# Optimization experiments

Hardware: AMD Instinct MI355X
Metric: run time of the kernel (lower is better)

## Reference

```python
import jax, jax.numpy as jnp
import numpy as np

N_QUBIT = 20
N_LAYER = 50
FEAT = 128
BATCH = 128
N_NODES = BATCH * N_QUBIT * (N_LAYER + 1)  # 130560
N_EDGES = 524288
VOCAB = N_QUBIT * (N_LAYER + 1) + 1  # 1021
NEG_SLOPE = 0.01


def setup_inputs() -> dict:
    key = jax.random.key(0)
    ks = jax.random.split(key, 32)
    s = 0.05
    x = jax.random.randint(ks[0], (N_NODES,), 0, VOCAB, dtype=jnp.int64 if jax.config.read('jax_enable_x64') else jnp.int32)
    edge_index = jax.random.randint(ks[1], (2, N_EDGES), 0, N_NODES, dtype=x.dtype)
    emb = (jax.random.normal(ks[2], (VOCAB, FEAT), jnp.float32) * s).at[0].set(0.0)  # padding_idx=0
    gcn_w = jax.random.normal(ks[3], (5, FEAT, FEAT), jnp.float32) * s
    gcn_b = jnp.zeros((5, FEAT), jnp.float32)
    mlp_dims = [(2 * FEAT, 2 * FEAT), (2 * FEAT, FEAT), (FEAT, FEAT), (FEAT, FEAT // 2), (FEAT // 2, FEAT // 2), (FEAT // 2, 1)]
    mlp = {}
    for i, (din, dout) in enumerate(mlp_dims):
        mlp[f'mw{i}'] = jax.random.normal(ks[4 + i], (din, dout), jnp.float32) * s
        mlp[f'mb{i}'] = jnp.zeros((dout,), jnp.float32)
    return dict(x=x, edge_index=edge_index, emb=emb, gcn_w=gcn_w, gcn_b=gcn_b, **mlp)


def _leaky(v):
    return jnp.where(v >= 0, v, NEG_SLOPE * v)


def _gcn(h, src, dst, W, b):
    # PyG GCNConv: h' = D^-1/2 (A+I) D^-1/2 (h W) + b, flow src -> dst
    n = h.shape[0]
    hw = h @ W
    loops = jnp.arange(n, dtype=src.dtype)
    s2 = jnp.concatenate([src, loops])
    d2 = jnp.concatenate([dst, loops])
    deg = jax.ops.segment_sum(jnp.ones(s2.shape[0], hw.dtype), d2, num_segments=n)
    dinv = jnp.where(deg > 0, jax.lax.rsqrt(deg), 0.0)
    norm = dinv[s2] * dinv[d2]  # [E+N]
    out = jax.ops.segment_sum(hw[s2] * norm[:, None], d2, num_segments=n)
    return out + b


def reference(x, edge_index, emb, gcn_w, gcn_b, mw0, mb0, mw1, mb1, mw2, mb2, mw3, mb3, mw4, mb4, mw5, mb5):
    src, dst = edge_index[0], edge_index[1]
    h = emb[x]  # [N, f]
    for i in range(4):
        h = _leaky(_gcn(h, src, dst, gcn_w[i], gcn_b[i])) + h
    h = _gcn(h, src, dst, gcn_w[4], gcn_b[4]) + h
    n, f = N_QUBIT, FEAT
    h = h.reshape(-1, n * (N_LAYER + 1), f)[:, :n, :]  # [B, n, f]
    b = h.shape[0]
    # cartesian pairs (i, j): concat(h_i, h_j) -> [B, n, n, 2f]
    xi = jnp.broadcast_to(h[:, :, None, :], (b, n, n, f))
    xj = jnp.broadcast_to(h[:, None, :, :], (b, n, n, f))
    p = jnp.concatenate([xi, xj], axis=-1)
    p = _leaky(p @ mw0 + mb0)
    p = _leaky(p @ mw1 + mb1)
    p = _leaky(p @ mw2 + mb2)
    p = _leaky(p @ mw3 + mb3)
    p = _leaky(p @ mw4 + mb4)
    p = (p @ mw5 + mb5)[..., 0]  # [B, n, n]
    p = (p + jnp.swapaxes(p, -1, -2)) / 2
    return p.reshape(-1, n * n)
```

## Files before the change

### kernel.cpp

```cpp
#include <hip/hip_runtime.h>
#include <hip/hip_bf16.h>

#define NQ 20
#define NLAY 51
#define FEAT 128
#define BATCH 128
#define NN (BATCH * NQ * NLAY)
#define NE 524288
#define NPAIR (BATCH * NQ * NQ)
#define NB (NN / 256)
#define VOCAB 1021

typedef _Float16 half8 __attribute__((ext_vector_type(8)));
typedef float floatx4 __attribute__((ext_vector_type(4)));
typedef unsigned int uint;

__device__ __forceinline__ float lrelu(float v) { return v >= 0.f ? v : 0.01f * v; }

__device__ __forceinline__ uint packhl(float v) {
    _Float16 h = (_Float16)v;
    _Float16 l = (_Float16)(v - (float)h);
    union { _Float16 f; unsigned short u; } hb, lb;
    hb.f = h; lb.f = l;
    return (uint)hb.u | ((uint)lb.u << 16);
}

__device__ __forceinline__ void unpack8(uint4 a, uint4 b, half8& hi, half8& lo) {
    union { uint u[4]; half8 h; } H, L;
    H.u[0] = __builtin_amdgcn_perm(a.y, a.x, 0x05040100u);
    H.u[1] = __builtin_amdgcn_perm(a.w, a.z, 0x05040100u);
    H.u[2] = __builtin_amdgcn_perm(b.y, b.x, 0x05040100u);
    H.u[3] = __builtin_amdgcn_perm(b.w, b.z, 0x05040100u);
    L.u[0] = __builtin_amdgcn_perm(a.y, a.x, 0x07060302u);
    L.u[1] = __builtin_amdgcn_perm(a.w, a.z, 0x07060302u);
    L.u[2] = __builtin_amdgcn_perm(b.y, b.x, 0x07060302u);
    L.u[3] = __builtin_amdgcn_perm(b.w, b.z, 0x07060302u);
    hi = H.h;
    lo = L.h;
}

__global__ void k_count(const int* __restrict__ dst, int* __restrict__ cnt) {
    int e = blockIdx.x * 256 + threadIdx.x;
    atomicAdd(&cnt[dst[e]], 1);
}

__global__ void k_offsets(const int* __restrict__ cnt, const int* __restrict__ x,
                          int* __restrict__ offs, float* __restrict__ dinv,
                          int4* __restrict__ meta, int* __restrict__ cursor,
                          int* __restrict__ flag1, int* __restrict__ idmap) {
    __shared__ int sm[256];
    __shared__ int sbase;
    int t = threadIdx.x, g = blockIdx.x * 256 + t;
    int v = cnt[g];
    sm[t] = v;
    __syncthreads();
    for (int s = 1; s < 256; s <<= 1) {
        int add = (t >= s) ? sm[t - s] : 0;
        __syncthreads();
        sm[t] += add;
        __syncthreads();
    }
    if (t == 255) sbase = atomicAdd(cursor, sm[255]);
    __syncthreads();
    int off = sbase + sm[t] - v;
    float di = rsqrtf((float)(v + 1));
    offs[g] = off;
    dinv[g] = di;
    meta[g] = make_int4(off, v, __float_as_int(di), x[g]);
    if (g % (NQ * NLAY) < NQ) flag1[g] = 1;
    if (g < 1024) idmap[g] = min(g, VOCAB - 1);
}

__global__ void k_fill(const int* __restrict__ src, const int* __restrict__ dst,
                       const int* __restrict__ offs, int* __restrict__ fill,
                       const float* __restrict__ dinv, const int* __restrict__ x,
                       int2* __restrict__ csre, int2* __restrict__ csre0,
                       int* __restrict__ flag1) {
    int e = blockIdx.x * 256 + threadIdx.x;
    int d = dst[e];
    int s = src[e];
    int pos = offs[d] + atomicAdd(&fill[d], 1);
    int wb = __float_as_int(dinv[s] * dinv[d]);
    csre[pos] = make_int2(s, wb);
    csre0[pos] = make_int2(x[s], wb);
    if (d % (NQ * NLAY) < NQ) flag1[s] = 1;
}

__global__ void k_s1pass(const int* __restrict__ flagI, const int4* __restrict__ meta,
                         const int2* __restrict__ csre, int* __restrict__ cur,
                         int* __restrict__ listO, int4* __restrict__ recO,
                         int* __restrict__ flagO) {
    __shared__ int sm[256];
    __shared__ int sbase;
    int t = threadIdx.x, g = blockIdx.x * 256 + t;
    int v = flagI[g];
    sm[t] = v;
    __syncthreads();
    for (int s = 1; s < 256; s <<= 1) {
        int add = (t >= s) ? sm[t - s] : 0;
        __syncthreads();
        sm[t] += add;
        __syncthreads();
    }
    if (t == 255) sbase = atomicAdd(cur, sm[255]);
    __syncthreads();
    if (v) {
        int slot = sbase + sm[t] - 1;
        listO[slot] = g;
        int4 m = meta[g];
        float di = __int_as_float(m.z);
        int dc = min(m.y, 6);
        int2 eb[6];
#pragma unroll
        for (int j = 0; j < 6; j++) eb[j] = (j < dc) ? csre[m.x + j] : make_int2(0, 0);
        int4* r = recO + (size_t)slot * 4;
        r[0] = make_int4(g + 1, m.y, __float_as_int(di * di), m.x);
        r[1] = make_int4(eb[0].x, eb[0].y, eb[1].x, eb[1].y);
        r[2] = make_int4(eb[2].x, eb[2].y, eb[3].x, eb[3].y);
        r[3] = make_int4(eb[4].x, eb[4].y, eb[5].x, eb[5].y);
        if (flagO) {
            flagO[g] = 1;
            for (int e = 0; e < m.y; e++) flagO[csre[m.x + e].x] = 1;
        }
    }
}

__global__ void k_rec0(const int4* __restrict__ meta, const int2* __restrict__ csre,
                       int4* __restrict__ rec0) {
    int q = blockIdx.x * 256 + threadIdx.x;
    if (q >= BATCH * NQ) return;
    int b = q / NQ, i = q - b * NQ;
    int node = b * (NQ * NLAY) + i;
    int4 m = meta[node];
    float di = __int_as_float(m.z);
    int dc = min(m.y, 6);
    int2 eb[6];
#pragma unroll
    for (int j = 0; j < 6; j++) eb[j] = (j < dc) ? csre[m.x + j] : make_int2(0, 0);
    int4* r = rec0 + (size_t)q * 4;
    r[0] = make_int4(node + 1, m.y, __float_as_int(di * di), m.x);
    r[1] = make_int4(eb[0].x, eb[0].y, eb[1].x, eb[1].y);
    r[2] = make_int4(eb[2].x, eb[2].y, eb[3].x, eb[3].y);
    r[3] = make_int4(eb[4].x, eb[4].y, eb[5].x, eb[5].y);
}

#define OFF_GCN 0
#define OFF_P0  81920
#define OFF_M1  147456
#define OFF_M2  180224
#define OFF_M3  196608
#define OFF_M4  204800
#define TS_TOTAL 208896

__global__ void k_tsplit_all(const float* __restrict__ gw, const float* __restrict__ mw0,
                             const float* __restrict__ mw1, const float* __restrict__ mw2,
                             const float* __restrict__ mw3, const float* __restrict__ mw4,
                             _Float16* __restrict__ hi, _Float16* __restrict__ lo) {
    int idx = blockIdx.x * 256 + threadIdx.x;
    const float* src;
    int K, N, rel;
    bool p0 = false;
    if (idx < OFF_P0) {
        int L = (idx - OFF_GCN) >> 14; rel = (idx - OFF_GCN) & 16383;
        src = gw + L * 16384; K = 128; N = 128;
    } else if (idx < OFF_M1) {
        rel = idx - OFF_P0; src = mw0; K = 128; N = 512; p0 = true;
    } else if (idx < OFF_M2) {
        rel = idx - OFF_M1;  src = mw1; K = 256; N = 128;
    } else if (idx < OFF_M3) {
        rel = idx - OFF_M2;  src = mw2; K = 128; N = 128;
    } else if (idx < OFF_M4) {
        rel = idx - OFF_M3;  src = mw3; K = 128; N = 64;
    } else {
        rel = idx - OFF_M4;  src = mw4; K = 64;  N = 64;
    }
    int kblks = K >> 5;
    int j = rel & 7;
    int lane = (rel >> 3) & 63;
    int t2 = rel >> 9;
    int kblk = t2 % kblks;
    int ntile = t2 / kblks;
    int col = ntile * 16 + (lane & 15);
    int k = kblk * 32 + ((lane >> 4) << 3) + j;
    float f;
    if (p0) {
        f = (col < 256) ? src[k * 256 + col] : src[(k + 128) * 256 + (col - 256)];
    } else {
        f = src[k * N + col];
    }
    _Float16 h = (_Float16)f;
    hi[idx] = h;
    lo[idx] = (_Float16)(f - (float)h);
}

template <int NT_N, bool LEAKY, bool BIAS, bool P0SPLIT, bool FUSEA, bool GATHA, bool LISTM>
__launch_bounds__(256, 2)
__global__ void hgemm(const float* __restrict__ A,
                      const float* __restrict__ FA, const float* __restrict__ FB,
                      const _Float16* __restrict__ Bh, const _Float16* __restrict__ Bl,
                      const float* __restrict__ bias,
                      float* __restrict__ C, float* __restrict__ C2,
                      int N, int K, const int* __restrict__ gmap,
                      const int* __restrict__ listm) {
    if (LISTM) {
        if ((unsigned)listm[blockIdx.x * 128] >= (unsigned)NN) return;
    }
    const int KB = K >> 5;
    const int lane = threadIdx.x & 63;
    const int wid = threadIdx.x >> 6;
    const int lm = lane & 15, lq = lane >> 4;
    const int m0 = blockIdx.x * 128 + wid * 32;
    const int n0t = blockIdx.y * NT_N;

    const float* arow[2];
    const float* brow[2];
#pragma unroll
    for (int mt = 0; mt < 2; mt++) {
        int row = m0 + mt * 16 + lm;
        if (FUSEA) {
            int b = row / (NQ * NQ);
            int rr = row - b * (NQ * NQ);
            int i = rr / NQ;
            int j = rr - i * NQ;
            arow[mt] = FA + (size_t)(b * NQ + i) * 256;
            brow[mt] = FB + (size_t)(b * NQ + j) * 256;
        } else if (GATHA) {
            arow[mt] = A + (size_t)gmap[row] * K;
        } else if (LISTM) {
            int lr = listm[row];
            lr = ((unsigned)lr < (unsigned)NN) ? lr : 0;
            arow[mt] = A + (size_t)lr * K;
        } else {
            arow[mt] = A + (size_t)row * K;
        }
    }

    floatx4 acc[2][NT_N];
#pragma unroll
    for (int mt = 0; mt < 2; mt++)
#pragma unroll
        for (int nt = 0; nt < NT_N; nt++) acc[mt][nt] = (floatx4)0.f;

    for (int kb = 0; kb < KB; kb++) {
        const int k0 = kb * 32 + lq * 8;
        half8 ahi[2], alo[2];
#pragma unroll
        for (int mt = 0; mt < 2; mt++) {
            floatx4 av0, av1;
            if (FUSEA) {
                floatx4 fa0 = *(const floatx4*)(arow[mt] + k0);
                floatx4 fa1 = *(const floatx4*)(arow[mt] + k0 + 4);
                floatx4 fb0 = *(const floatx4*)(brow[mt] + k0);
                floatx4 fb1 = *(const floatx4*)(brow[mt] + k0 + 4);
#pragma unroll
                for (int q = 0; q < 4; q++) {
                    av0[q] = lrelu(fa0[q] + fb0[q]);
                    av1[q] = lrelu(fa1[q] + fb1[q]);
                }
            } else {
                av0 = *(const floatx4*)(arow[mt] + k0);
                av1 = *(const floatx4*)(arow[mt] + k0 + 4);
            }
#pragma unroll
            for (int q = 0; q < 4; q++) {
                _Float16 h0 = (_Float16)av0[q];
                ahi[mt][q] = h0;
                alo[mt][q] = (_Float16)(av0[q] - (float)h0);
                _Float16 h1 = (_Float16)av1[q];
                ahi[mt][4 + q] = h1;
                alo[mt][4 + q] = (_Float16)(av1[q] - (float)h1);
            }
        }
#pragma unroll
        for (int nt = 0; nt < NT_N; nt++) {
            size_t boff = (((size_t)(n0t + nt) * KB + kb) * 64 + lane) * 8;
            half8 bhi = *(const half8*)(Bh + boff);
            half8 blo = *(const half8*)(Bl + boff);
#pragma unroll
            for (int mt = 0; mt < 2; mt++) {
                acc[mt][nt] = __builtin_amdgcn_mfma_f32_16x16x32_f16(ahi[mt], bhi, acc[mt][nt], 0, 0, 0);
                acc[mt][nt] = __builtin_amdgcn_mfma_f32_16x16x32_f16(ahi[mt], blo, acc[mt][nt], 0, 0, 0);
                acc[mt][nt] = __builtin_amdgcn_mfma_f32_16x16x32_f16(alo[mt], bhi, acc[mt][nt], 0, 0, 0);
            }
        }
    }

    int strow[2][4];
    bool svalid[2][4];
#pragma unroll
    for (int mt = 0; mt < 2; mt++)
#pragma unroll
        for (int r = 0; r < 4; r++) {
            int mlog = m0 + mt * 16 + lq * 4 + r;
            if (LISTM) {
                int sr = listm[mlog];
                svalid[mt][r] = (unsigned)sr < (unsigned)NN;
                strow[mt][r] = svalid[mt][r] ? sr : 0;
            } else {
                svalid[mt][r] = true;
                strow[mt][r] = mlog;
            }
        }

#pragma unroll
    for (int nt = 0; nt < NT_N; nt++) {
        int col = (n0t + nt) * 16 + lm;
        float bv = (BIAS || P0SPLIT) ? bias[col < 256 ? col : 0] : 0.f;
#pragma unroll
        for (int mt = 0; mt < 2; mt++) {
#pragma unroll
            for (int r = 0; r < 4; r++) {
                if (!svalid[mt][r]) continue;
                int row = strow[mt][r];
                float val = acc[mt][nt][r];
                if (P0SPLIT) {
                    if (col < 256) C[(size_t)row * 256 + col] = val + bv;
                    else C2[(size_t)row * 256 + col - 256] = val;
                } else {
                    if (BIAS) val += bv;
                    if (LEAKY) val = lrelu(val);
                    C[(size_t)row * N + col] = val;
                }
            }
        }
    }
}

template <bool LEAKY, bool FINAL>
__launch_bounds__(256, 8)
__global__ void k_lagg(const float* __restrict__ in, float* __restrict__ outp,
                       const int4* __restrict__ rec, const int2* __restrict__ csre,
                       const int* __restrict__ cntp, int fixcnt,
                       const _Float16* __restrict__ Bh, const _Float16* __restrict__ Bl,
                       const float* __restrict__ bias) {
    int lcnt = cntp ? *cntp : fixcnt;
    int sbase = blockIdx.x * 16;
    if (sbase >= lcnt) return;
    __shared__ uint X[16][132];
    int tid = threadIdx.x;
    int sl = tid & 31;
    int grp = tid >> 5;
    const float4* in4 = (const float4*)in;
    {
        int lrow0 = grp * 2;
        int p0i = sbase + lrow0, p1i = p0i + 1;
        bool val0 = p0i < lcnt, val1 = p1i < lcnt;
        const int4* r0p = rec + (size_t)(val0 ? p0i : 0) * 4;
        const int4* r1p = rec + (size_t)(val1 ? p1i : 0) * 4;
        int4 hd0 = r0p[0], ea0 = r0p[1], eb0 = r0p[2], ec0 = r0p[3];
        int4 hd1 = r1p[0], ea1 = r1p[1], eb1 = r1p[2], ec1 = r1p[3];
        int n0 = hd0.x - 1;
        int n1 = hd1.x - 1;
        float s20 = __int_as_float(hd0.z), s21 = __int_as_float(hd1.z);
        float4 v0  = in4[(size_t)n0 * 32 + sl];
        float4 v1  = in4[(size_t)n1 * 32 + sl];
        float4 u00 = in4[(size_t)ea0.x * 32 + sl];
        float4 u01 = in4[(size_t)ea0.z * 32 + sl];
        float4 u02 = in4[(size_t)eb0.x * 32 + sl];
        float4 u03 = in4[(size_t)eb0.z * 32 + sl];
        float4 u04 = in4[(size_t)ec0.x * 32 + sl];
        float4 u05 = in4[(size_t)ec0.z * 32 + sl];
        float4 u10 = in4[(size_t)ea1.x * 32 + sl];
        float4 u11 = in4[(size_t)ea1.z * 32 + sl];
        float4 u12 = in4[(size_t)eb1.x * 32 + sl];
        float4 u13 = in4[(size_t)eb1.z * 32 + sl];
        float4 u14 = in4[(size_t)ec1.x * 32 + sl];
        float4 u15 = in4[(size_t)ec1.z * 32 + sl];
        float w00 = __int_as_float(ea0.y), w01 = __int_as_float(ea0.w);
        float w02 = __int_as_float(eb0.y), w03 = __int_as_float(eb0.w);
        float w04 = __int_as_float(ec0.y), w05 = __int_as_float(ec0.w);
        float w10 = __int_as_float(ea1.y), w11 = __int_as_float(ea1.w);
        float w12 = __int_as_float(eb1.y), w13 = __int_as_float(eb1.w);
        float w14 = __int_as_float(ec1.y), w15 = __int_as_float(ec1.w);
        float a0x = v0.x * s20 + u00.x * w00 + u01.x * w01 + u02.x * w02 + u03.x * w03 + u04.x * w04 + u05.x * w05;
        float a0y = v0.y * s20 + u00.y * w00 + u01.y * w01 + u02.y * w02 + u03.y * w03 + u04.y * w04 + u05.y * w05;
        float a0z = v0.z * s20 + u00.z * w00 + u01.z * w01 + u02.z * w02 + u03.z * w03 + u04.z * w04 + u05.z * w05;
        float a0w = v0.w * s20 + u00.w * w00 + u01.w * w01 + u02.w * w02 + u03.w * w03 + u04.w * w04 + u05.w * w05;
        float a1x = v1.x * s21 + u10.x * w10 + u11.x * w11 + u12.x * w12 + u13.x * w13 + u14.x * w14 + u15.x * w15;
        float a1y = v1.y * s21 + u10.y * w10 + u11.y * w11 + u12.y * w12 + u13.y * w13 + u14.y * w14 + u15.y * w15;
        float a1z = v1.z * s21 + u10.z * w10 + u11.z * w11 + u12.z * w12 + u13.z * w13 + u14.z * w14 + u15.z * w15;
        float a1w = v1.w * s21 + u10.w * w10 + u11.w * w11 + u12.w * w12 + u13.w * w13 + u14.w * w14 + u15.w * w15;
        int deg0 = val0 ? hd0.y : 0, deg1 = val1 ? hd1.y : 0;
        int dm = max(deg0, deg1);
        if (dm > 6) {
            int off0 = hd0.w, off1 = hd1.w;
            int d0c = max(deg0 - 1, 0), d1c = max(deg1 - 1, 0);
            for (int e = 6; e < dm; e += 6) {
                int2 e00 = csre[off0 + min(e,     d0c)];
                int2 e01 = csre[off0 + min(e + 1, d0c)];
                int2 e02 = csre[off0 + min(e + 2, d0c)];
                int2 e03 = csre[off0 + min(e + 3, d0c)];
                int2 e04 = csre[off0 + min(e + 4, d0c)];
                int2 e05 = csre[off0 + min(e + 5, d0c)];
                int2 e10 = csre[off1 + min(e,     d1c)];
                int2 e11 = csre[off1 + min(e + 1, d1c)];
                int2 e12 = csre[off1 + min(e + 2, d1c)];
                int2 e13 = csre[off1 + min(e + 3, d1c)];
                int2 e14 = csre[off1 + min(e + 4, d1c)];
                int2 e15 = csre[off1 + min(e + 5, d1c)];
                float4 x00 = in4[(size_t)e00.x * 32 + sl];
                float4 x01 = in4[(size_t)e01.x * 32 + sl];
                float4 x02 = in4[(size_t)e02.x * 32 + sl];
                float4 x03 = in4[(size_t)e03.x * 32 + sl];
                float4 x04 = in4[(size_t)e04.x * 32 + sl];
                float4 x05 = in4[(size_t)e05.x * 32 + sl];
                float4 x10 = in4[(size_t)e10.x * 32 + sl];
                float4 x11 = in4[(size_t)e11.x * 32 + sl];
                float4 x12 = in4[(size_t)e12.x * 32 + sl];
                float4 x13 = in4[(size_t)e13.x * 32 + sl];
                float4 x14 = in4[(size_t)e14.x * 32 + sl];
                float4 x15 = in4[(size_t)e15.x * 32 + sl];
                float q00 = (e     < deg0) ? __int_as_float(e00.y) : 0.f;
                float q01 = (e + 1 < deg0) ? __int_as_float(e01.y) : 0.f;
                float q02 = (e + 2 < deg0) ? __int_as_float(e02.y) : 0.f;
                float q03 = (e + 3 < deg0) ? __int_as_float(e03.y) : 0.f;
                float q04 = (e + 4 < deg0) ? __int_as_float(e04.y) : 0.f;
                float q05 = (e + 5 < deg0) ? __int_as_float(e05.y) : 0.f;
                float q10 = (e     < deg1) ? __int_as_float(e10.y) : 0.f;
                float q11 = (e + 1 < deg1) ? __int_as_float(e11.y) : 0.f;
                float q12 = (e + 2 < deg1) ? __int_as_float(e12.y) : 0.f;
                float q13 = (e + 3 < deg1) ? __int_as_float(e13.y) : 0.f;
                float q14 = (e + 4 < deg1) ? __int_as_float(e14.y) : 0.f;
                float q15 = (e + 5 < deg1) ? __int_as_float(e15.y) : 0.f;
                a0x += x00.x * q00 + x01.x * q01 + x02.x * q02 + x03.x * q03 + x04.x * q04 + x05.x * q05;
                a0y += x00.y * q00 + x01.y * q01 + x02.y * q02 + x03.y * q03 + x04.y * q04 + x05.y * q05;
                a0z += x00.z * q00 + x01.z * q01 + x02.z * q02 + x03.z * q03 + x04.z * q04 + x05.z * q05;
                a0w += x00.w * q00 + x01.w * q01 + x02.w * q02 + x03.w * q03 + x04.w * q04 + x05.w * q05;
                a1x += x10.x * q10 + x11.x * q11 + x12.x * q12 + x13.x * q13 + x14.x * q14 + x15.x * q15;
                a1y += x10.y * q10 + x11.y * q11 + x12.y * q12 + x13.y * q13 + x14.y * q14 + x15.y * q15;
                a1z += x10.z * q10 + x11.z * q11 + x12.z * q12 + x13.z * q13 + x14.z * q14 + x15.z * q15;
                a1w += x10.w * q10 + x11.w * q11 + x12.w * q12 + x13.w * q13 + x14.w * q14 + x15.w * q15;
            }
        }
        *(uint4*)&X[lrow0][sl * 4] =
            make_uint4(packhl(a0x), packhl(a0y), packhl(a0z), packhl(a0w));
        *(uint4*)&X[lrow0 + 1][sl * 4] =
            make_uint4(packhl(a1x), packhl(a1y), packhl(a1z), packhl(a1w));
    }
    __syncthreads();
    const int lane = tid & 63;
    const int wid = tid >> 6;
    const int lm = lane & 15, lq = lane >> 4;
    floatx4 acc[2];
    acc[0] = (floatx4)0.f;
    acc[1] = (floatx4)0.f;
#pragma unroll
    for (int kb = 0; kb < 4; kb++) {
        const int k0 = kb * 32 + lq * 8;
        uint4 pa = *(const uint4*)&X[lm][k0];
        uint4 pb = *(const uint4*)&X[lm][k0 + 4];
        half8 ahi, alo;
        unpack8(pa, pb, ahi, alo);
#pragma unroll
        for (int ntl = 0; ntl < 2; ntl++) {
            int nt = wid * 2 + ntl;
            size_t boff = (((size_t)nt * 4 + kb) * 64 + lane) * 8;
            half8 bhi = *(const half8*)(Bh + boff);
            half8 blo = *(const half8*)(Bl + boff);
            acc[ntl] = __builtin_amdgcn_mfma_f32_16x16x32_f16(ahi, bhi, acc[ntl], 0, 0, 0);
            acc[ntl] = __builtin_amdgcn_mfma_f32_16x16x32_f16(ahi, blo, acc[ntl], 0, 0, 0);
            acc[ntl] = __builtin_amdgcn_mfma_f32_16x16x32_f16(alo, bhi, acc[ntl], 0, 0, 0);
        }
    }
    int nodes[4];
    bool sval[4];
#pragma unroll
    for (int r = 0; r < 4; r++) {
        int slot = sbase + lq * 4 + r;
        sval[r] = slot < lcnt;
        nodes[r] = sval[r] ? (rec[(size_t)slot * 4].x - 1) : 0;
    }
#pragma unroll
    for (int ntl = 0; ntl < 2; ntl++) {
        int col = (wid * 2 + ntl) * 16 + lm;
        float bv = bias[col];
#pragma unroll
        for (int r = 0; r < 4; r++) {
            if (!sval[r]) continue;
            float val = acc[ntl][r] + bv;
            if (LEAKY) val = lrelu(val);
            val += in[(size_t)nodes[r] * FEAT + col];
            if (FINAL)
                outp[(size_t)(sbase + lq * 4 + r) * FEAT + col] = val;
            else
                outp[(size_t)nodes[r] * FEAT + col] = val;
        }
    }
}

template <int KB, int NT>
__device__ __forceinline__ void pair_stage(uint (*__restrict__ X)[132],
                                           const _Float16* __restrict__ Bh,
                                           const _Float16* __restrict__ Bl,
                                           const float* __restrict__ bias,
                                           int srow, int lane) {
    const int lm = lane & 15, lq = lane >> 4;
    floatx4 acc[NT];
#pragma unroll
    for (int nt = 0; nt < NT; nt++) acc[nt] = (floatx4)0.f;
#pragma unroll
    for (int kb = 0; kb < KB; kb++) {
        const int k0 = kb * 32 + lq * 8;
        uint4 pa = *(const uint4*)&X[srow + lm][k0];
        uint4 pb = *(const uint4*)&X[srow + lm][k0 + 4];
        half8 ahi, alo;
        unpack8(pa, pb, ahi, alo);
#pragma unroll
        for (int nt = 0; nt < NT; nt++) {
            size_t boff = (((size_t)nt * KB + kb) * 64 + lane) * 8;
            half8 bhi = *(const half8*)(Bh + boff);
            half8 blo = *(const half8*)(Bl + boff);
            acc[nt] = __builtin_amdgcn_mfma_f32_16x16x32_f16(ahi, bhi, acc[nt], 0, 0, 0);
            acc[nt] = __builtin_amdgcn_mfma_f32_16x16x32_f16(ahi, blo, acc[nt], 0, 0, 0);
            acc[nt] = __builtin_amdgcn_mfma_f32_16x16x32_f16(alo, bhi, acc[nt], 0, 0, 0);
        }
    }
#pragma unroll
    for (int nt = 0; nt < NT; nt++) {
        int col = nt * 16 + lm;
        float bv = bias[col];
#pragma unroll
        for (int r = 0; r < 4; r++) {
            X[srow + lq * 4 + r][col] = packhl(lrelu(acc[nt][r] + bv));
        }
    }
}

__launch_bounds__(256, 4)
__global__ void k_pair(const float* __restrict__ FA, const float* __restrict__ FB,
                       const _Float16* __restrict__ bth, const _Float16* __restrict__ btl,
                       const float* __restrict__ mb1, const float* __restrict__ mb2,
                       const float* __restrict__ mb3, const float* __restrict__ mb4,
                       const float* __restrict__ mw5, const float* __restrict__ mb5,
                       float* __restrict__ sbuf) {
    __shared__ uint X[64][132];
    const int lane = threadIdx.x & 63;
    const int wid = threadIdx.x >> 6;
    const int lm = lane & 15, lq = lane >> 4;
    const int srow = wid * 16;
    const int rbase = blockIdx.x * 64;

    {
        const int grow = rbase + srow + lm;
        int b = grow / (NQ * NQ);
        int rr = grow - b * (NQ * NQ);
        int i = rr / NQ;
        int j = rr - i * NQ;
        const float* arow = FA + (size_t)(b * NQ + i) * 256;
        const float* brow = FB + (size_t)(b * NQ + j) * 256;
        const _Float16* Bh = bth + OFF_M1;
        const _Float16* Bl = btl + OFF_M1;
        floatx4 acc[8];
#pragma unroll
        for (int nt = 0; nt < 8; nt++) acc[nt] = (floatx4)0.f;
        const int KB = 8;
#pragma unroll
        for (int kb = 0; kb < KB; kb++) {
            const int k0 = kb * 32 + lq * 8;
            floatx4 fa0 = *(const floatx4*)(arow + k0);
            floatx4 fa1 = *(const floatx4*)(arow + k0 + 4);
            floatx4 fb0 = *(const floatx4*)(brow + k0);
            floatx4 fb1 = *(const floatx4*)(brow + k0 + 4);
            half8 ahi, alo;
#pragma unroll
            for (int q = 0; q < 4; q++) {
                float v0 = lrelu(fa0[q] + fb0[q]);
                float v1 = lrelu(fa1[q] + fb1[q]);
                _Float16 h0 = (_Float16)v0;
                ahi[q] = h0;
                alo[q] = (_Float16)(v0 - (float)h0);
                _Float16 h1 = (_Float16)v1;
                ahi[4 + q] = h1;
                alo[4 + q] = (_Float16)(v1 - (float)h1);
            }
#pragma unroll
            for (int nt = 0; nt < 8; nt++) {
                size_t boff = (((size_t)nt * KB + kb) * 64 + lane) * 8;
                half8 bhi = *(const half8*)(Bh + boff);
                half8 blo = *(const half8*)(Bl + boff);
                acc[nt] = __builtin_amdgcn_mfma_f32_16x16x32_f16(ahi, bhi, acc[nt], 0, 0, 0);
                acc[nt] = __builtin_amdgcn_mfma_f32_16x16x32_f16(ahi, blo, acc[nt], 0, 0, 0);
                acc[nt] = __builtin_amdgcn_mfma_f32_16x16x32_f16(alo, bhi, acc[nt], 0, 0, 0);
            }
        }
#pragma unroll
        for (int nt = 0; nt < 8; nt++) {
            int col = nt * 16 + lm;
            float bv = mb1[col];
#pragma unroll
            for (int r = 0; r < 4; r++) {
                X[srow + lq * 4 + r][col] = packhl(lrelu(acc[nt][r] + bv));
            }
        }
    }
    pair_stage<4, 8>(X, bth + OFF_M2, btl + OFF_M2, mb2, srow, lane);
    pair_stage<4, 4>(X, bth + OFF_M3, btl + OFF_M3, mb3, srow, lane);
    pair_stage<2, 4>(X, bth + OFF_M4, btl + OFF_M4, mb4, srow, lane);
    {
        int row = srow + (lane >> 2);
        int part = lane & 3;
        float s = 0.f;
#pragma unroll
        for (int c4 = 0; c4 < 4; c4++) {
            int c0 = part * 16 + c4 * 4;
            uint4 u = *(const uint4*)&X[row][c0];
            const float* wp = mw5 + c0;
            uint uu[4] = {u.x, u.y, u.z, u.w};
#pragma unroll
            for (int q = 0; q < 4; q++) {
                union { unsigned short us; _Float16 f; } ch, cl;
                ch.us = (unsigned short)(uu[q] & 0xffffu);
                cl.us = (unsigned short)(uu[q] >> 16);
                s += ((float)ch.f + (float)cl.f) * wp[q];
            }
        }
        s += __shfl_xor(s, 1);
        s += __shfl_xor(s, 2);
        if (part == 0) sbuf[rbase + row] = s + mb5[0];
    }
}

__global__ void k_sym(const float* __restrict__ sbuf, float* __restrict__ out) {
    int p = blockIdx.x * 256 + threadIdx.x;
    int b = p / (NQ * NQ);
    int rr = p - b * (NQ * NQ);
    int i = rr / NQ, j = rr - i * NQ;
    float a = sbuf[p];
    float c = sbuf[b * (NQ * NQ) + j * NQ + i];
    out[p] = 0.5f * (a + c);
}

__global__ void k_agg0(const float* __restrict__ embW, const float* __restrict__ emb,
                       float* __restrict__ h,
                       const int4* __restrict__ meta, const int2* __restrict__ csre0,
                       const float* __restrict__ bias) {
    int tid = threadIdx.x;
    int sl = tid & 31;
    int p = blockIdx.x * 8 + (tid >> 5);
    int n0 = p * 2, n1 = n0 + 1;
    int4 m0 = meta[n0], m1 = meta[n1];
    float di0 = __int_as_float(m0.z), di1 = __int_as_float(m1.z);
    int off0 = m0.x, deg0 = m0.y;
    int off1 = m1.x, deg1 = m1.y;
    float4 v0 = ((const float4*)(embW + (size_t)m0.w * FEAT))[sl];
    float4 v1 = ((const float4*)(embW + (size_t)m1.w * FEAT))[sl];
    float4 ho0 = ((const float4*)(emb + (size_t)m0.w * FEAT))[sl];
    float4 ho1 = ((const float4*)(emb + (size_t)m1.w * FEAT))[sl];
    float s20 = di0 * di0, s21 = di1 * di1;
    float a0x = v0.x * s20, a0y = v0.y * s20, a0z = v0.z * s20, a0w = v0.w * s20;
    float a1x = v1.x * s21, a1y = v1.y * s21, a1z = v1.z * s21, a1w = v1.w * s21;
    int d0c = max(deg0 - 1, 0), d1c = max(deg1 - 1, 0);
    int dm = max(deg0, deg1);
    for (int e = 0; e < dm; e += 4) {
        int2 e00 = csre0[off0 + min(e,     d0c)];
        int2 e01 = csre0[off0 + min(e + 1, d0c)];
        int2 e02 = csre0[off0 + min(e + 2, d0c)];
        int2 e03 = csre0[off0 + min(e + 3, d0c)];
        int2 e10 = csre0[off1 + min(e,     d1c)];
        int2 e11 = csre0[off1 + min(e + 1, d1c)];
        int2 e12 = csre0[off1 + min(e + 2, d1c)];
        int2 e13 = csre0[off1 + min(e + 3, d1c)];
        float4 u00 = ((const float4*)(embW + (size_t)e00.x * FEAT))[sl];
        float4 u01 = ((const float4*)(embW + (size_t)e01.x * FEAT))[sl];
        float4 u02 = ((const float4*)(embW + (size_t)e02.x * FEAT))[sl];
        float4 u03 = ((const float4*)(embW + (size_t)e03.x * FEAT))[sl];
        float4 u10 = ((const float4*)(embW + (size_t)e10.x * FEAT))[sl];
        float4 u11 = ((const float4*)(embW + (size_t)e11.x * FEAT))[sl];
        float4 u12 = ((const float4*)(embW + (size_t)e12.x * FEAT))[sl];
        float4 u13 = ((const float4*)(embW + (size_t)e13.x * FEAT))[sl];
        float w00 = (e     < deg0) ? __int_as_float(e00.y) : 0.f;
        float w01 = (e + 1 < deg0) ? __int_as_float(e01.y) : 0.f;
        float w02 = (e + 2 < deg0) ? __int_as_float(e02.y) : 0.f;
        float w03 = (e + 3 < deg0) ? __int_as_float(e03.y) : 0.f;
        float w10 = (e     < deg1) ? __int_as_float(e10.y) : 0.f;
        float w11 = (e + 1 < deg1) ? __int_as_float(e11.y) : 0.f;
        float w12 = (e + 2 < deg1) ? __int_as_float(e12.y) : 0.f;
        float w13 = (e + 3 < deg1) ? __int_as_float(e13.y) : 0.f;
        a0x += u00.x * w00 + u01.x * w01 + u02.x * w02 + u03.x * w03;
        a0y += u00.y * w00 + u01.y * w01 + u02.y * w02 + u03.y * w03;
        a0z += u00.z * w00 + u01.z * w01 + u02.z * w02 + u03.z * w03;
        a0w += u00.w * w00 + u01.w * w01 + u02.w * w02 + u03.w * w03;
        a1x += u10.x * w10 + u11.x * w11 + u12.x * w12 + u13.x * w13;
        a1y += u10.y * w10 + u11.y * w11 + u12.y * w12 + u13.y * w13;
        a1z += u10.z * w10 + u11.z * w11 + u12.z * w12 + u13.z * w13;
        a1w += u10.w * w10 + u11.w * w11 + u12.w * w12 + u13.w * w13;
    }
    float4 bv = ((const float4*)bias)[sl];
    float4 r0, r1;
    r0.x = lrelu(a0x + bv.x) + ho0.x;
    r0.y = lrelu(a0y + bv.y) + ho0.y;
    r0.z = lrelu(a0z + bv.z) + ho0.z;
    r0.w = lrelu(a0w + bv.w) + ho0.w;
    r1.x = lrelu(a1x + bv.x) + ho1.x;
    r1.y = lrelu(a1y + bv.y) + ho1.y;
    r1.z = lrelu(a1z + bv.z) + ho1.z;
    r1.w = lrelu(a1w + bv.w) + ho1.w;
    ((float4*)(h + (size_t)n0 * FEAT))[sl] = r0;
    ((float4*)(h + (size_t)n1 * FEAT))[sl] = r1;
}

extern "C" void kernel_launch(void* const* d_in, const int* in_sizes, int n_in,
                              void* d_out, int out_size, void* d_ws, size_t ws_size,
                              hipStream_t stream) {
    const int* x = (const int*)d_in[0];
    const int* ei = (const int*)d_in[1];
    const int* e_src = ei;
    const int* e_dst = ei + NE;
    const float* emb = (const float*)d_in[2];
    const float* gw = (const float*)d_in[3];
    const float* gb = (const float*)d_in[4];
    const float* mw0 = (const float*)d_in[5];
    const float* mb0 = (const float*)d_in[6];
    const float* mw1 = (const float*)d_in[7];
    const float* mb1 = (const float*)d_in[8];
    const float* mw2 = (const float*)d_in[9];
    const float* mb2 = (const float*)d_in[10];
    const float* mw3 = (const float*)d_in[11];
    const float* mb3 = (const float*)d_in[12];
    const float* mw4 = (const float*)d_in[13];
    const float* mb4 = (const float*)d_in[14];
    const float* mw5 = (const float*)d_in[15];
    const float* mb5 = (const float*)d_in[16];
    float* out = (float*)d_out;

    float* wsf = (float*)d_ws;
    size_t o = 0;
    const size_t HSZ = (size_t)NN * FEAT;
    float* h  = wsf + o; o += HSZ;
    float* hw = wsf + o; o += HSZ;
    int* cnt   = (int*)(wsf + o); o += NN;
    int* fill  = (int*)(wsf + o); o += NN;
    int* flag1 = (int*)(wsf + o); o += NN;
    int* flag2 = (int*)(wsf + o); o += NN;
    int* flag3 = (int*)(wsf + o); o += NN;
    int* curs  = (int*)(wsf + o); o += 16;
    int* list1 = (int*)(wsf + o); o += NN;
    int* list2 = (int*)(wsf + o); o += NN;
    int* list3 = (int*)(wsf + o); o += NN;
    int* offs = (int*)(wsf + o); o += NN;
    float* dinv = wsf + o; o += NN;
    int4* meta = (int4*)(wsf + o); o += 4 * (size_t)NN;
    int2* csre  = (int2*)(wsf + o); o += 2 * (size_t)(NE + 8);
    int2* csre0 = (int2*)(wsf + o); o += 2 * (size_t)(NE + 8);
    int* idmap = (int*)(wsf + o); o += 1024;
    float* embW = wsf + o; o += (size_t)1024 * FEAT;
    float* hq = wsf + o; o += (size_t)BATCH * NQ * FEAT;
    float* Abuf = wsf + o; o += (size_t)BATCH * NQ * 256;
    float* Bbuf = wsf + o; o += (size_t)BATCH * NQ * 256;
    int4* rec1 = (int4*)(wsf + o); o += 16 * (size_t)NN;
    int4* rec2 = (int4*)(wsf + o); o += 16 * (size_t)NN;
    int4* rec3 = (int4*)(wsf + o); o += 16 * (size_t)NN;
    int4* rec0 = (int4*)(wsf + o); o += 16 * (size_t)(BATCH * NQ);
    _Float16* bt_hi = (_Float16*)(wsf + o); o += (TS_TOTAL + 2) / 2;
    _Float16* bt_lo = (_Float16*)(wsf + o); o += (TS_TOTAL + 2) / 2;
    float* sbuf = hw;

    k_tsplit_all<<<TS_TOTAL / 256, 256, 0, stream>>>(gw, mw0, mw1, mw2, mw3, mw4, bt_hi, bt_lo);

    hipMemsetAsync(cnt, 0, (5 * NN + 16) * sizeof(int), stream);
    hipMemsetAsync(csre + NE, 0, 8 * sizeof(int2), stream);
    hipMemsetAsync(csre0 + NE, 0, 8 * sizeof(int2), stream);
    k_count<<<NE / 256, 256, 0, stream>>>(e_dst, cnt);
    k_offsets<<<NB, 256, 0, stream>>>(cnt, x, offs, dinv, meta, curs + 0, flag1, idmap);
    k_fill<<<NE / 256, 256, 0, stream>>>(e_src, e_dst, offs, fill, dinv, x, csre, csre0, flag1);
    k_rec0<<<(BATCH * NQ + 255) / 256, 256, 0, stream>>>(meta, csre, rec0);
    k_s1pass<<<NB, 256, 0, stream>>>(flag1, meta, csre, curs + 1, list1, rec1, flag2);
    k_s1pass<<<NB, 256, 0, stream>>>(flag2, meta, csre, curs + 2, list2, rec2, flag3);
    k_s1pass<<<NB, 256, 0, stream>>>(flag3, meta, csre, curs + 3, list3, rec3, nullptr);

    hgemm<1, false, false, false, false, true, false><<<dim3(8, 8), 256, 0, stream>>>(
        emb, nullptr, nullptr, bt_hi + OFF_GCN, bt_lo + OFF_GCN,
        nullptr, embW, nullptr, FEAT, FEAT, idmap, nullptr);
    k_agg0<<<NN / 16, 256, 0, stream>>>(embW, emb, h, meta, csre0, gb + 0 * FEAT);

    k_lagg<true, false><<<NN / 16, 256, 0, stream>>>(
        h, hw, rec3, csre, curs + 3, 0,
        bt_hi + OFF_GCN + 1 * 16384, bt_lo + OFF_GCN + 1 * 16384, gb + 1 * FEAT);
    k_lagg<true, false><<<NN / 16, 256, 0, stream>>>(
        hw, h, rec2, csre, curs + 2, 0,
        bt_hi + OFF_GCN + 2 * 16384, bt_lo + OFF_GCN + 2 * 16384, gb + 2 * FEAT);
    k_lagg<true, false><<<NN / 16, 256, 0, stream>>>(
        h, hw, rec1, csre, curs + 1, 0,
        bt_hi + OFF_GCN + 3 * 16384, bt_lo + OFF_GCN + 3 * 16384, gb + 3 * FEAT);
    k_lagg<false, true><<<(BATCH * NQ) / 16, 256, 0, stream>>>(
        hw, hq, rec0, csre, nullptr, BATCH * NQ,
        bt_hi + OFF_GCN + 4 * 16384, bt_lo + OFF_GCN + 4 * 16384, gb + 4 * FEAT);

    hgemm<2, false, false, true, false, false, false><<<dim3(20, 16), 256, 0, stream>>>(
        hq, nullptr, nullptr, bt_hi + OFF_P0, bt_lo + OFF_P0, mb0, Abuf, Bbuf, 512, 128,
        nullptr, nullptr);
    k_pair<<<NPAIR / 64, 256, 0, stream>>>(Abuf, Bbuf, bt_hi, bt_lo,
                                           mb1, mb2, mb3, mb4, mw5, mb5, sbuf);
    k_sym<<<NPAIR / 256, 256, 0, stream>>>(sbuf, out);
}
```

Measured before the change: 403.0 us.

## Precompute per-node edge records, edge-parallel flag marking, reuse residual from LDS

Flag propagation for the frontier passes moves from a serial per-node loop inside the scan kernel into a separate edge-parallel marking kernel, and the unused node lists are dropped. A new pass builds padded 6-edge records for all nodes so the first aggregation does the first six neighbors without a dependent CSR walk, looping only for higher degrees. The layer kernel keeps each self-row in shared memory and reads the residual from there instead of reloading it from global memory. This adds two extra edge-sized launches, one full-size record buffer, and extra LDS per block that may lower occupancy.

```diff
diff --git a/kernel.cpp b/kernel.cpp
--- a/kernel.cpp
+++ b/kernel.cpp
@@ -86,10 +86,15 @@
     if (d % (NQ * NLAY) < NQ) flag1[s] = 1;
 }
 
+__global__ void k_mark(const int* __restrict__ src, const int* __restrict__ dst,
+                       const int* __restrict__ flagI, int* __restrict__ flagO) {
+    int e = blockIdx.x * 256 + threadIdx.x;
+    if (flagI[dst[e]]) flagO[src[e]] = 1;
+}
+
 __global__ void k_s1pass(const int* __restrict__ flagI, const int4* __restrict__ meta,
                          const int2* __restrict__ csre, int* __restrict__ cur,
-                         int* __restrict__ listO, int4* __restrict__ recO,
-                         int* __restrict__ flagO) {
+                         int4* __restrict__ recO, int* __restrict__ flagO) {
     __shared__ int sm[256];
     __shared__ int sbase;
     int t = threadIdx.x, g = blockIdx.x * 256 + t;
@@ -106,7 +111,6 @@
     __syncthreads();
     if (v) {
         int slot = sbase + sm[t] - 1;
-        listO[slot] = g;
         int4 m = meta[g];
         float di = __int_as_float(m.z);
         int dc = min(m.y, 6);
@@ -118,10 +122,7 @@
         r[1] = make_int4(eb[0].x, eb[0].y, eb[1].x, eb[1].y);
         r[2] = make_int4(eb[2].x, eb[2].y, eb[3].x, eb[3].y);
         r[3] = make_int4(eb[4].x, eb[4].y, eb[5].x, eb[5].y);
-        if (flagO) {
-            flagO[g] = 1;
-            for (int e = 0; e < m.y; e++) flagO[csre[m.x + e].x] = 1;
-        }
+        if (flagO) flagO[g] = 1;
     }
 }
 
@@ -139,6 +140,22 @@
     for (int j = 0; j < 6; j++) eb[j] = (j < dc) ? csre[m.x + j] : make_int2(0, 0);
     int4* r = rec0 + (size_t)q * 4;
     r[0] = make_int4(node + 1, m.y, __float_as_int(di * di), m.x);
+    r[1] = make_int4(eb[0].x, eb[0].y, eb[1].x, eb[1].y);
+    r[2] = make_int4(eb[2].x, eb[2].y, eb[3].x, eb[3].y);
+    r[3] = make_int4(eb[4].x, eb[4].y, eb[5].x, eb[5].y);
+}
+
+__global__ void k_recall(const int4* __restrict__ meta, const int2* __restrict__ csre0,
+                         int4* __restrict__ recT) {
+    int g = blockIdx.x * 256 + threadIdx.x;
+    int4 m = meta[g];
+    float di = __int_as_float(m.z);
+    int dc = min(m.y, 6);
+    int2 eb[6];
+#pragma unroll
+    for (int j = 0; j < 6; j++) eb[j] = (j < dc) ? csre0[m.x + j] : make_int2(0, 0);
+    int4* r = recT + (size_t)g * 4;
+    r[0] = make_int4(m.w, m.y, __float_as_int(di * di), m.x);
     r[1] = make_int4(eb[0].x, eb[0].y, eb[1].x, eb[1].y);
     r[2] = make_int4(eb[2].x, eb[2].y, eb[3].x, eb[3].y);
     r[3] = make_int4(eb[4].x, eb[4].y, eb[5].x, eb[5].y);
@@ -337,6 +354,7 @@
     int sbase = blockIdx.x * 16;
     if (sbase >= lcnt) return;
     __shared__ uint X[16][132];
+    __shared__ float R[16][132];
     int tid = threadIdx.x;
     int sl = tid & 31;
     int grp = tid >> 5;
@@ -366,6 +384,8 @@
         float4 u13 = in4[(size_t)eb1.z * 32 + sl];
         float4 u14 = in4[(size_t)ec1.x * 32 + sl];
         float4 u15 = in4[(size_t)ec1.z * 32 + sl];
+        *(float4*)&R[lrow0][sl * 4] = v0;
+        *(float4*)&R[lrow0 + 1][sl * 4] = v1;
         float w00 = __int_as_float(ea0.y), w01 = __int_as_float(ea0.w);
         float w02 = __int_as_float(eb0.y), w03 = __int_as_float(eb0.w);
         float w04 = __int_as_float(ec0.y), w05 = __int_as_float(ec0.w);
@@ -479,7 +499,7 @@
             if (!sval[r]) continue;
             float val = acc[ntl][r] + bv;
             if (LEAKY) val = lrelu(val);
-            val += in[(size_t)nodes[r] * FEAT + col];
+            val += R[lq * 4 + r][col];
             if (FINAL)
                 outp[(size_t)(sbase + lq * 4 + r) * FEAT + col] = val;
             else
@@ -631,59 +651,100 @@
 }
 
 __global__ void k_agg0(const float* __restrict__ embW, const float* __restrict__ emb,
-                       float* __restrict__ h,
-                       const int4* __restrict__ meta, const int2* __restrict__ csre0,
-                       const float* __restrict__ bias) {
+                       float* __restrict__ h, const int4* __restrict__ recT,
+                       const int2* __restrict__ csre0, const float* __restrict__ bias) {
     int tid = threadIdx.x;
     int sl = tid & 31;
     int p = blockIdx.x * 8 + (tid >> 5);
     int n0 = p * 2, n1 = n0 + 1;
-    int4 m0 = meta[n0], m1 = meta[n1];
-    float di0 = __int_as_float(m0.z), di1 = __int_as_float(m1.z);
-    int off0 = m0.x, deg0 = m0.y;
-    int off1 = m1.x, deg1 = m1.y;
-    float4 v0 = ((const float4*)(embW + (size_t)m0.w * FEAT))[sl];
-    float4 v1 = ((const float4*)(embW + (size_t)m1.w * FEAT))[sl];
-    float4 ho0 = ((const float4*)(emb + (size_t)m0.w * FEAT))[sl];
-    float4 ho1 = ((const float4*)(emb + (size_t)m1.w * FEAT))[sl];
-    float s20 = di0 * di0, s21 = di1 * di1;
-    float a0x = v0.x * s20, a0y = v0.y * s20, a0z = v0.z * s20, a0w = v0.w * s20;
-    float a1x = v1.x * s21, a1y = v1.y * s21, a1z = v1.z * s21, a1w = v1.w * s21;
-    int d0c = max(deg0 - 1, 0), d1c = max(deg1 - 1, 0);
+    const int4* r0p = recT + (size_t)n0 * 4;
+    const int4* r1p = recT + (size_t)n1 * 4;
+    int4 hd0 = r0p[0], ea0 = r0p[1], eb0 = r0p[2], ec0 = r0p[3];
+    int4 hd1 = r1p[0], ea1 = r1p[1], eb1 = r1p[2], ec1 = r1p[3];
+    int t0 = hd0.x, t1 = hd1.x;
+    float s20 = __int_as_float(hd0.z), s21 = __int_as_float(hd1.z);
+    const float4* w4 = (const float4*)embW;
+    float4 v0  = w4[(size_t)t0 * 32 + sl];
+    float4 v1  = w4[(size_t)t1 * 32 + sl];
+    float4 u00 = w4[(size_t)ea0.x * 32 + sl];
+    float4 u01 = w4[(size_t)ea0.z * 32 + sl];
+    float4 u02 = w4[(size_t)eb0.x * 32 + sl];
+    float4 u03 = w4[(size_t)eb0.z * 32 + sl];
+    float4 u04 = w4[(size_t)ec0.x * 32 + sl];
+    float4 u05 = w4[(size_t)ec0.z * 32 + sl];
+    float4 u10 = w4[(size_t)ea1.x * 32 + sl];
+    float4 u11 = w4[(size_t)ea1.z * 32 + sl];
+    float4 u12 = w4[(size_t)eb1.x * 32 + sl];
+    float4 u13 = w4[(size_t)eb1.z * 32 + sl];
+    float4 u14 = w4[(size_t)ec1.x * 32 + sl];
+    float4 u15 = w4[(size_t)ec1.z * 32 + sl];
+    float4 ho0 = ((const float4*)emb)[(size_t)t0 * 32 + sl];
+    float4 ho1 = ((const float4*)emb)[(size_t)t1 * 32 + sl];
+    float w00 = __int_as_float(ea0.y), w01 = __int_as_float(ea0.w);
+    float w02 = __int_as_float(eb0.y), w03 = __int_as_float(eb0.w);
+    float w04 = __int_as_float(ec0.y), w05 = __int_as_float(ec0.w);
+    float w10 = __int_as_float(ea1.y), w11 = __int_as_float(ea1.w);
+    float w12 = __int_as_float(eb1.y), w13 = __int_as_float(eb1.w);
+    float w14 = __int_as_float(ec1.y), w15 = __int_as_float(ec1.w);
+    float a0x = v0.x * s20 + u00.x * w00 + u01.x * w01 + u02.x * w02 + u03.x * w03 + u04.x * w04 + u05.x * w05;
+    float a0y = v0.y * s20 + u00.y * w00 + u01.y * w01 + u02.y * w02 + u03.y * w03 + u04.y * w04 + u05.y * w05;
+    float a0z = v0.z * s20 + u00.z * w00 + u01.z * w01 + u02.z * w02 + u03.z * w03 + u04.z * w04 + u05.z * w05;
+    float a0w = v0.w * s20 + u00.w * w00 + u01.w * w01 + u02.w * w02 + u03.w * w03 + u04.w * w04 + u05.w * w05;
+    float a1x = v1.x * s21 + u10.x * w10 + u11.x * w11 + u12.x * w12 + u13.x * w13 + u14.x * w14 + u15.x * w15;
+    float a1y = v1.y * s21 + u10.y * w10 + u11.y * w11 + u12.y * w12 + u13.y * w13 + u14.y * w14 + u15.y * w15;
+    float a1z = v1.z * s21 + u10.z * w10 + u11.z * w11 + u12.z * w12 + u13.z * w13 + u14.z * w14 + u15.z * w15;
+    float a1w = v1.w * s21 + u10.w * w10 + u11.w * w11 + u12.w * w12 + u13.w * w13 + u14.w * w14 + u15.w * w15;
+    int deg0 = hd0.y, deg1 = hd1.y;
     int dm = max(deg0, deg1);
-    for (int e = 0; e < dm; e += 4) {
-        int2 e00 = csre0[off0 + min(e,     d0c)];
-        int2 e01 = csre0[off0 + min(e + 1, d0c)];
-        int2 e02 = csre0[off0 + min(e + 2, d0c)];
-        int2 e03 = csre0[off0 + min(e + 3, d0c)];
-        int2 e10 = csre0[off1 + min(e,     d1c)];
-        int2 e11 = csre0[off1 + min(e + 1, d1c)];
-        int2 e12 = csre0[off1 + min(e + 2, d1c)];
-        int2 e13 = csre0[off1 + min(e + 3, d1c)];
-        float4 u00 = ((const float4*)(embW + (size_t)e00.x * FEAT))[sl];
-        float4 u01 = ((const float4*)(embW + (size_t)e01.x * FEAT))[sl];
-        float4 u02 = ((const float4*)(embW + (size_t)e02.x * FEAT))[sl];
-        float4 u03 = ((const float4*)(embW + (size_t)e03.x * FEAT))[sl];
-        float4 u10 = ((const float4*)(embW + (size_t)e10.x * FEAT))[sl];
-        float4 u11 = ((const float4*)(embW + (size_t)e11.x * FEAT))[sl];
-        float4 u12 = ((const float4*)(embW + (size_t)e12.x * FEAT))[sl];
-        float4 u13 = ((const float4*)(embW + (size_t)e13.x * FEAT))[sl];
-        float w00 = (e     < deg0) ? __int_as_float(e00.y) : 0.f;
-        float w01 = (e + 1 < deg0) ? __int_as_float(e01.y) : 0.f;
-        float w02 = (e + 2 < deg0) ? __int_as_float(e02.y) : 0.f;
-        float w03 = (e + 3 < deg0) ? __int_as_float(e03.y) : 0.f;
-        float w10 = (e     < deg1) ? __int_as_float(e10.y) : 0.f;
-        float w11 = (e + 1 < deg1) ? __int_as_float(e11.y) : 0.f;
-        float w12 = (e + 2 < deg1) ? __int_as_float(e12.y) : 0.f;
-        float w13 = (e + 3 < deg1) ? __int_as_float(e13.y) : 0.f;
-        a0x += u00.x * w00 + u01.x * w01 + u02.x * w02 + u03.x * w03;
-        a0y += u00.y * w00 + u01.y * w01 + u02.y * w02 + u03.y * w03;
-        a0z += u00.z * w00 + u01.z * w01 + u02.z * w02 + u03.z * w03;
-        a0w += u00.w * w00 + u01.w * w01 + u02.w * w02 + u03.w * w03;
-        a1x += u10.x * w10 + u11.x * w11 + u12.x * w12 + u13.x * w13;
-        a1y += u10.y * w10 + u11.y * w11 + u12.y * w12 + u13.y * w13;
-        a1z += u10.z * w10 + u11.z * w11 + u12.z * w12 + u13.z * w13;
-        a1w += u10.w * w10 + u11.w * w11 + u12.w * w12 + u13.w * w13;
+    if (dm > 6) {
+        int off0 = hd0.w, off1 = hd1.w;
+        int d0c = max(deg0 - 1, 0), d1c = max(deg1 - 1, 0);
+        for (int e = 6; e < dm; e += 6) {
+            int2 e00 = csre0[off0 + min(e,     d0c)];
+            int2 e01 = csre0[off0 + min(e + 1, d0c)];
+            int2 e02 = csre0[off0 + min(e + 2, d0c)];
+            int2 e03 = csre0[off0 + min(e + 3, d0c)];
+            int2 e04 = csre0[off0 + min(e + 4, d0c)];
+            int2 e05 = csre0[off0 + min(e + 5, d0c)];
+            int2 e10 = csre0[off1 + min(e,     d1c)];
+            int2 e11 = csre0[off1 + min(e + 1, d1c)];
+            int2 e12 = csre0[off1 + min(e + 2, d1c)];
+            int2 e13 = csre0[off1 + min(e + 3, d1c)];
+            int2 e14 = csre0[off1 + min(e + 4, d1c)];
+            int2 e15 = csre0[off1 + min(e + 5, d1c)];
+            float4 x00 = w4[(size_t)e00.x * 32 + sl];
+            float4 x01 = w4[(size_t)e01.x * 32 + sl];
+            float4 x02 = w4[(size_t)e02.x * 32 + sl];
+            float4 x03 = w4[(size_t)e03.x * 32 + sl];
+            float4 x04 = w4[(size_t)e04.x * 32 + sl];
+            float4 x05 = w4[(size_t)e05.x * 32 + sl];
+            float4 x10 = w4[(size_t)e10.x * 32 + sl];
+            float4 x11 = w4[(size_t)e11.x * 32 + sl];
+            float4 x12 = w4[(size_t)e12.x * 32 + sl];
+            float4 x13 = w4[(size_t)e13.x * 32 + sl];
+            float4 x14 = w4[(size_t)e14.x * 32 + sl];
+            float4 x15 = w4[(size_t)e15.x * 32 + sl];
+            float q00 = (e     < deg0) ? __int_as_float(e00.y) : 0.f;
+            float q01 = (e + 1 < deg0) ? __int_as_float(e01.y) : 0.f;
+            float q02 = (e + 2 < deg0) ? __int_as_float(e02.y) : 0.f;
+            float q03 = (e + 3 < deg0) ? __int_as_float(e03.y) : 0.f;
+            float q04 = (e + 4 < deg0) ? __int_as_float(e04.y) : 0.f;
+            float q05 = (e + 5 < deg0) ? __int_as_float(e05.y) : 0.f;
+            float q10 = (e     < deg1) ? __int_as_float(e10.y) : 0.f;
+            float q11 = (e + 1 < deg1) ? __int_as_float(e11.y) : 0.f;
+            float q12 = (e + 2 < deg1) ? __int_as_float(e12.y) : 0.f;
+            float q13 = (e + 3 < deg1) ? __int_as_float(e13.y) : 0.f;
+            float q14 = (e + 4 < deg1) ? __int_as_float(e14.y) : 0.f;
+            float q15 = (e + 5 < deg1) ? __int_as_float(e15.y) : 0.f;
+            a0x += x00.x * q00 + x01.x * q01 + x02.x * q02 + x03.x * q03 + x04.x * q04 + x05.x * q05;
+            a0y += x00.y * q00 + x01.y * q01 + x02.y * q02 + x03.y * q03 + x04.y * q04 + x05.y * q05;
+            a0z += x00.z * q00 + x01.z * q01 + x02.z * q02 + x03.z * q03 + x04.z * q04 + x05.z * q05;
+            a0w += x00.w * q00 + x01.w * q01 + x02.w * q02 + x03.w * q03 + x04.w * q04 + x05.w * q05;
+            a1x += x10.x * q10 + x11.x * q11 + x12.x * q12 + x13.x * q13 + x14.x * q14 + x15.x * q15;
+            a1y += x10.y * q10 + x11.y * q11 + x12.y * q12 + x13.y * q13 + x14.y * q14 + x15.y * q15;
+            a1z += x10.z * q10 + x11.z * q11 + x12.z * q12 + x13.z * q13 + x14.z * q14 + x15.z * q15;
+            a1w += x10.w * q10 + x11.w * q11 + x12.w * q12 + x13.w * q13 + x14.w * q14 + x15.w * q15;
+        }
     }
     float4 bv = ((const float4*)bias)[sl];
     float4 r0, r1;
@@ -734,9 +795,6 @@
     int* flag2 = (int*)(wsf + o); o += NN;
     int* flag3 = (int*)(wsf + o); o += NN;
     int* curs  = (int*)(wsf + o); o += 16;
-    int* list1 = (int*)(wsf + o); o += NN;
-    int* list2 = (int*)(wsf + o); o += NN;
-    int* list3 = (int*)(wsf + o); o += NN;
     int* offs = (int*)(wsf + o); o += NN;
     float* dinv = wsf + o; o += NN;
     int4* meta = (int4*)(wsf + o); o += 4 * (size_t)NN;
@@ -750,6 +808,7 @@
     int4* rec1 = (int4*)(wsf + o); o += 16 * (size_t)NN;
     int4* rec2 = (int4*)(wsf + o); o += 16 * (size_t)NN;
     int4* rec3 = (int4*)(wsf + o); o += 16 * (size_t)NN;
+    int4* recT = (int4*)(wsf + o); o += 16 * (size_t)NN;
     int4* rec0 = (int4*)(wsf + o); o += 16 * (size_t)(BATCH * NQ);
     _Float16* bt_hi = (_Float16*)(wsf + o); o += (TS_TOTAL + 2) / 2;
     _Float16* bt_lo = (_Float16*)(wsf + o); o += (TS_TOTAL + 2) / 2;
@@ -763,15 +822,18 @@
     k_count<<<NE / 256, 256, 0, stream>>>(e_dst, cnt);
     k_offsets<<<NB, 256, 0, stream>>>(cnt, x, offs, dinv, meta, curs + 0, flag1, idmap);
     k_fill<<<NE / 256, 256, 0, stream>>>(e_src, e_dst, offs, fill, dinv, x, csre, csre0, flag1);
+    k_recall<<<NB, 256, 0, stream>>>(meta, csre0, recT);
     k_rec0<<<(BATCH * NQ + 255) / 256, 256, 0, stream>>>(meta, csre, rec0);
-    k_s1pass<<<NB, 256, 0, stream>>>(flag1, meta, csre, curs + 1, list1, rec1, flag2);
-    k_s1pass<<<NB, 256, 0, stream>>>(flag2, meta, csre, curs + 2, list2, rec2, flag3);
-    k_s1pass<<<NB, 256, 0, stream>>>(flag3, meta, csre, curs + 3, list3, rec3, nullptr);
+    k_s1pass<<<NB, 256, 0, stream>>>(flag1, meta, csre, curs + 1, rec1, flag2);
+    k_mark<<<NE / 256, 256, 0, stream>>>(e_src, e_dst, flag1, flag2);
+    k_s1pass<<<NB, 256, 0, stream>>>(flag2, meta, csre, curs + 2, rec2, flag3);
+    k_mark<<<NE / 256, 256, 0, stream>>>(e_src, e_dst, flag2, flag3);
+    k_s1pass<<<NB, 256, 0, stream>>>(flag3, meta, csre, curs + 3, rec3, nullptr);
 
     hgemm<1, false, false, false, false, true, false><<<dim3(8, 8), 256, 0, stream>>>(
         emb, nullptr, nullptr, bt_hi + OFF_GCN, bt_lo + OFF_GCN,
         nullptr, embW, nullptr, FEAT, FEAT, idmap, nullptr);
-    k_agg0<<<NN / 16, 256, 0, stream>>>(embW, emb, h, meta, csre0, gb + 0 * FEAT);
+    k_agg0<<<NN / 16, 256, 0, stream>>>(embW, emb, h, recT, csre0, gb + 0 * FEAT);
 
     k_lagg<true, false><<<NN / 16, 256, 0, stream>>>(
         h, hw, rec3, csre, curs + 3, 0,
```

New measurement: 404.4 us. Within noise of the previous version (+0.4%).
